# Kernel tuning notes

Measured on AMD Instinct MI355X. Metric: run time of the kernel, lower is better.

Reference implementation:

```python
import jax, jax.numpy as jnp
import numpy as np

PZ = 8            # pz half-patch in get_dist_base
P = 2 * PZ        # patch side = 16
C, T, HF, WF = 128, 3, 256, 256
N = 2048          # number of keypoint pairs


def setup_inputs() -> dict:
    key = jax.random.key(0)
    ks = jax.random.split(key, 9)
    response = jax.random.normal(ks[0], (C, T, HF, WF), dtype=jnp.float32)
    ys1 = jax.random.randint(ks[1], (N,), 0, HF - P, dtype=jnp.int32)
    xs1 = jax.random.randint(ks[2], (N,), 0, WF - P, dtype=jnp.int32)
    ts1 = jax.random.randint(ks[3], (N,), 0, T, dtype=jnp.int32)
    ys2 = jax.random.randint(ks[4], (N,), 0, HF - P, dtype=jnp.int32)
    xs2 = jax.random.randint(ks[5], (N,), 0, WF - P, dtype=jnp.int32)
    ts2 = jax.random.randint(ks[6], (N,), 0, T, dtype=jnp.int32)
    pair_type = jax.random.randint(ks[7], (N,), 0, 3, dtype=jnp.int32)  # 0=BG,1=I,2=IS
    powers = 1.0 + jax.random.uniform(ks[8], (3,), dtype=jnp.float32)   # per-type exponent in [1,2)
    plus = jnp.ones((1,), dtype=jnp.float32)
    return dict(response=response, ys1=ys1, xs1=xs1, ts1=ts1,
                ys2=ys2, xs2=xs2, ts2=ts2, pair_type=pair_type,
                powers=powers, plus=plus)


def _gather_patches(response, ts, ys, xs):
    # response: [C, T, Hf, Wf] -> patches [N, C, P, P]
    c = response.shape[0]
    def one(t, y, x):
        return jax.lax.dynamic_slice(response, (0, t, y, x), (c, 1, P, P))[:, 0]
    return jax.vmap(one)(ts, ys, xs)


def _minmax_norm(p):
    # normalize_tensor: min-max over whole patch; identity if max==min
    mn = p.min(axis=(1, 2, 3), keepdims=True)
    mx = p.max(axis=(1, 2, 3), keepdims=True)
    rng = mx - mn
    return jnp.where(rng != 0, (p - mn) / jnp.where(rng == 0, 1.0, rng), p)


def reference(response, ys1, xs1, ts1, ys2, xs2, ts2, pair_type, powers, plus):
    P1 = _minmax_norm(_gather_patches(response, ts1, ys1, xs1))
    P2 = _minmax_norm(_gather_patches(response, ts2, ys2, xs2))
    pw = powers[pair_type][:, None, None, None]            # per-pair exponent
    d = jnp.mean(jnp.abs(P1 - P2) ** pw, axis=(1, 2, 3))   # losscal core, [N]
    per = jnp.where(pair_type == 2, d, 1.0 / (1.0 + d))    # IS -> losscal_1, BG/I -> losscal_2
    per = per + jnp.where(pair_type == 0, 0.0, plus[0] * 0.5)  # + plus/2 for I and IS
    return jnp.mean(per)                                   # lossbase / act
```

## Files before the change

### kernel.cpp

```cpp
#include <hip/hip_runtime.h>
#include <math.h>

#define CC 128
#define TT 3
#define HFD 256
#define WFD 256
#define PP 16
#define NPAIR 2048
#define HW (HFD * WFD)
#define POS (TT * HW)
#define CH_STRIDE POS
#define PATCH_ELEMS (CC * PP * PP)
#define BLOCK 256
#define TP 256

typedef float floatx2 __attribute__((ext_vector_type(2)));
typedef float floatx4 __attribute__((ext_vector_type(4)));

__global__ __launch_bounds__(BLOCK) void transpose_minmax_kernel(
    const float* __restrict__ resp,
    unsigned int* __restrict__ rt32,
    float* __restrict__ cmn, float* __restrict__ cmx) {
    __shared__ unsigned int tile32[TP][33];
    __shared__ float smn[4][TP], smx[4][TP];

    int p0 = blockIdx.x * TP;
    int pc = threadIdx.x & 63;
    int ph = threadIdx.x >> 6;

    const float* bp = resp + p0 + 4 * pc;

    float mn0 = INFINITY, mn1 = INFINITY, mn2 = INFINITY, mn3 = INFINITY;
    float mx0 = -INFINITY, mx1 = -INFINITY, mx2 = -INFINITY, mx3 = -INFINITY;

    #pragma unroll
    for (int k = 0; k < 8; ++k) {
        int q = k * 4 + ph;
        floatx4 l0 = *(const floatx4*)(bp + (size_t)(4 * q + 0) * CH_STRIDE);
        floatx4 l1 = *(const floatx4*)(bp + (size_t)(4 * q + 1) * CH_STRIDE);
        floatx4 l2 = *(const floatx4*)(bp + (size_t)(4 * q + 2) * CH_STRIDE);
        floatx4 l3 = *(const floatx4*)(bp + (size_t)(4 * q + 3) * CH_STRIDE);
        #pragma unroll
        for (int j = 0; j < 4; ++j) {
            float v0 = l0[j], v1 = l1[j], v2 = l2[j], v3 = l3[j];
            float mnj = fminf(fminf(v0, v1), fminf(v2, v3));
            float mxj = fmaxf(fmaxf(v0, v1), fmaxf(v2, v3));
            if (j == 0) { mn0 = fminf(mn0, mnj); mx0 = fmaxf(mx0, mxj); }
            if (j == 1) { mn1 = fminf(mn1, mnj); mx1 = fmaxf(mx1, mxj); }
            if (j == 2) { mn2 = fminf(mn2, mnj); mx2 = fmaxf(mx2, mxj); }
            if (j == 3) { mn3 = fminf(mn3, mnj); mx3 = fmaxf(mx3, mxj); }
            int w = __builtin_amdgcn_cvt_pk_fp8_f32(v0, v1, 0, false);
            w = __builtin_amdgcn_cvt_pk_fp8_f32(v2, v3, w, true);
            tile32[4 * pc + j][q] = (unsigned int)w;
        }
    }
    smn[ph][4 * pc + 0] = mn0; smx[ph][4 * pc + 0] = mx0;
    smn[ph][4 * pc + 1] = mn1; smx[ph][4 * pc + 1] = mx1;
    smn[ph][4 * pc + 2] = mn2; smx[ph][4 * pc + 2] = mx2;
    smn[ph][4 * pc + 3] = mn3; smx[ph][4 * pc + 3] = mx3;
    __syncthreads();

    int tp = threadIdx.x;
    cmn[p0 + tp] = fminf(fminf(smn[0][tp], smn[1][tp]), fminf(smn[2][tp], smn[3][tp]));
    cmx[p0 + tp] = fmaxf(fmaxf(smx[0][tp], smx[1][tp]), fmaxf(smx[2][tp], smx[3][tp]));

    #pragma unroll
    for (int j = 0; j < 32; ++j) {
        int u   = j * BLOCK + threadIdx.x;
        int pos = u >> 5;
        int c4  = u & 31;
        rt32[(((size_t)(p0 + pos)) << 5) + c4] = tile32[pos][c4];
    }
}

__device__ inline float pw_term(float va, float vb, float sc1, float nsc2, float K, float pw) {
    float d = fmaf(va, sc1, fmaf(vb, nsc2, K));
    return __builtin_amdgcn_exp2f(pw * __builtin_amdgcn_logf(fabsf(d)));
}

__device__ inline float quad_acc(unsigned int wa, unsigned int wb,
                                 float sc1, float nsc2, float K, float pw) {
    floatx2 a0 = __builtin_amdgcn_cvt_pk_f32_fp8((int)wa, false);
    floatx2 a1 = __builtin_amdgcn_cvt_pk_f32_fp8((int)wa, true);
    floatx2 b0 = __builtin_amdgcn_cvt_pk_f32_fp8((int)wb, false);
    floatx2 b1 = __builtin_amdgcn_cvt_pk_f32_fp8((int)wb, true);
    return pw_term(a0.x, b0.x, sc1, nsc2, K, pw) + pw_term(a0.y, b0.y, sc1, nsc2, K, pw)
         + pw_term(a1.x, b1.x, sc1, nsc2, K, pw) + pw_term(a1.y, b1.y, sc1, nsc2, K, pw);
}

__global__ __launch_bounds__(BLOCK) void pair_loss_kernel(
    const uint4* __restrict__ rt,
    const int* __restrict__ ts1, const int* __restrict__ ys1, const int* __restrict__ xs1,
    const int* __restrict__ ts2, const int* __restrict__ ys2, const int* __restrict__ xs2,
    const int* __restrict__ pair_type,
    const float* __restrict__ powers,
    const float* __restrict__ plus,
    const float* __restrict__ cmn, const float* __restrict__ cmx,
    float* __restrict__ per_out) {
    int i = blockIdx.x;
    int t1 = ts1[i], y1 = ys1[i], x1 = xs1[i];
    int t2 = ts2[i], y2 = ys2[i], x2 = xs2[i];
    int p1 = t1 * HW + y1 * WFD + x1;
    int p2 = t2 * HW + y2 * WFD + x2;

    int dy = threadIdx.x >> 4, dx = threadIdx.x & 15;
    int q1 = p1 + dy * WFD + dx;
    int q2 = p2 + dy * WFD + dx;
    float a0 = cmn[q1], a1 = cmx[q1];
    float b0 = cmn[q2], b1 = cmx[q2];
    #pragma unroll
    for (int off = 32; off > 0; off >>= 1) {
        a0 = fminf(a0, __shfl_down(a0, off));
        a1 = fmaxf(a1, __shfl_down(a1, off));
        b0 = fminf(b0, __shfl_down(b0, off));
        b1 = fmaxf(b1, __shfl_down(b1, off));
    }
    __shared__ float red[4][4];
    int wave = threadIdx.x >> 6;
    if ((threadIdx.x & 63) == 0) {
        red[wave][0] = a0; red[wave][1] = a1; red[wave][2] = b0; red[wave][3] = b1;
    }
    __syncthreads();
    float mn1 = fminf(fminf(red[0][0], red[1][0]), fminf(red[2][0], red[3][0]));
    float mx1 = fmaxf(fmaxf(red[0][1], red[1][1]), fmaxf(red[2][1], red[3][1]));
    float mn2 = fminf(fminf(red[0][2], red[1][2]), fminf(red[2][2], red[3][2]));
    float mx2 = fmaxf(fmaxf(red[0][3], red[1][3]), fmaxf(red[2][3], red[3][3]));

    float rg1 = mx1 - mn1, rg2 = mx2 - mn2;
    float sc1 = (rg1 != 0.0f) ? (1.0f / rg1) : 1.0f;
    float sh1 = (rg1 != 0.0f) ? mn1 : 0.0f;
    float sc2 = (rg2 != 0.0f) ? (1.0f / rg2) : 1.0f;
    float sh2 = (rg2 != 0.0f) ? mn2 : 0.0f;
    float nsc2 = -sc2;
    float K = sh2 * sc2 - sh1 * sc1;

    int   ptype = pair_type[i];
    float pw    = powers[ptype];

    int c16 = threadIdx.x & 7;
    int pdx = (threadIdx.x >> 3) & 15;
    int dyb = threadIdx.x >> 7;
    const uint4* A = rt + (((size_t)(p1 + pdx)) << 3) + c16;
    const uint4* B = rt + (((size_t)(p2 + pdx)) << 3) + c16;
    const size_t RSTR = (size_t)WFD << 3;

    float acc = 0.0f;
    #pragma unroll
    for (int j = 0; j < 8; ++j) {
        size_t off = (size_t)(dyb + 2 * j) * RSTR;
        uint4 wa = A[off];
        uint4 wb = B[off];
        acc += quad_acc(wa.x, wb.x, sc1, nsc2, K, pw);
        acc += quad_acc(wa.y, wb.y, sc1, nsc2, K, pw);
        acc += quad_acc(wa.z, wb.z, sc1, nsc2, K, pw);
        acc += quad_acc(wa.w, wb.w, sc1, nsc2, K, pw);
    }
    for (int off = 32; off > 0; off >>= 1) acc += __shfl_down(acc, off);
    __shared__ float ssum[BLOCK / 64];
    if ((threadIdx.x & 63) == 0) ssum[wave] = acc;
    __syncthreads();
    if (threadIdx.x == 0) {
        float total = ssum[0] + ssum[1] + ssum[2] + ssum[3];
        float dmean = total * (1.0f / (float)PATCH_ELEMS);
        float per = (ptype == 2) ? dmean : (1.0f / (1.0f + dmean));
        per += (ptype == 0) ? 0.0f : plus[0] * 0.5f;
        per_out[i] = per;
    }
}

__global__ __launch_bounds__(BLOCK) void final_mean_kernel(
    const float* __restrict__ per_out, float* __restrict__ out) {
    float acc = 0.0f;
    for (int i = threadIdx.x; i < NPAIR; i += BLOCK) acc += per_out[i];
    for (int off = 32; off > 0; off >>= 1) acc += __shfl_down(acc, off);
    __shared__ float ssum[BLOCK / 64];
    int wave = threadIdx.x >> 6;
    if ((threadIdx.x & 63) == 0) ssum[wave] = acc;
    __syncthreads();
    if (threadIdx.x == 0) {
        float total = ssum[0] + ssum[1] + ssum[2] + ssum[3];
        out[0] = total * (1.0f / (float)NPAIR);
    }
}

extern "C" void kernel_launch(void* const* d_in, const int* in_sizes, int n_in,
                              void* d_out, int out_size, void* d_ws, size_t ws_size,
                              hipStream_t stream) {
    const float* resp      = (const float*)d_in[0];
    const int*   ys1       = (const int*)d_in[1];
    const int*   xs1       = (const int*)d_in[2];
    const int*   ts1       = (const int*)d_in[3];
    const int*   ys2       = (const int*)d_in[4];
    const int*   xs2       = (const int*)d_in[5];
    const int*   ts2       = (const int*)d_in[6];
    const int*   pair_type = (const int*)d_in[7];
    const float* powers    = (const float*)d_in[8];
    const float* plus      = (const float*)d_in[9];
    float*       out       = (float*)d_out;

    unsigned int* rt32 = (unsigned int*)d_ws;
    float* cmn     = (float*)(rt32 + (size_t)POS * 32);
    float* cmx     = cmn + POS;
    float* per_out = cmx + POS;

    transpose_minmax_kernel<<<POS / TP, BLOCK, 0, stream>>>(resp, rt32, cmn, cmx);

    pair_loss_kernel<<<NPAIR, BLOCK, 0, stream>>>(
        (const uint4*)rt32, ts1, ys1, xs1, ts2, ys2, xs2, pair_type, powers, plus,
        cmn, cmx, per_out);

    final_mean_kernel<<<1, BLOCK, 0, stream>>>(per_out, out);
}
```

Before: 192.6 us.

## Split pair blocks in half, shrink transpose tile, hoist loads, precompute powers

The transpose/minmax kernel now works on 128-position tiles, which doubles its block count and gives each thread fewer channel loads. The pair kernel launches two blocks per pair, each covering half the patch rows. Each block issues its patch loads before the min/max reduction, with a sched barrier to keep them early. Per-pair exponents are precomputed by a small extra kernel, and the final per-pair combine moves into the final mean kernel. A stray dead load of cmn is left in, and the extra launch and partial-sum traffic add overhead.

```diff
diff --git a/kernel.cpp b/kernel.cpp
--- a/kernel.cpp
+++ b/kernel.cpp
@@ -12,7 +12,7 @@
 #define CH_STRIDE POS
 #define PATCH_ELEMS (CC * PP * PP)
 #define BLOCK 256
-#define TP 256
+#define TP 128
 
 typedef float floatx2 __attribute__((ext_vector_type(2)));
 typedef float floatx4 __attribute__((ext_vector_type(4)));
@@ -22,11 +22,11 @@
     unsigned int* __restrict__ rt32,
     float* __restrict__ cmn, float* __restrict__ cmx) {
     __shared__ unsigned int tile32[TP][33];
-    __shared__ float smn[4][TP], smx[4][TP];
+    __shared__ float smn[8][TP], smx[8][TP];
 
     int p0 = blockIdx.x * TP;
-    int pc = threadIdx.x & 63;
-    int ph = threadIdx.x >> 6;
+    int pc = threadIdx.x & 31;
+    int ph = threadIdx.x >> 5;
 
     const float* bp = resp + p0 + 4 * pc;
 
@@ -34,8 +34,8 @@
     float mx0 = -INFINITY, mx1 = -INFINITY, mx2 = -INFINITY, mx3 = -INFINITY;
 
     #pragma unroll
-    for (int k = 0; k < 8; ++k) {
-        int q = k * 4 + ph;
+    for (int k = 0; k < 4; ++k) {
+        int q = k * 8 + ph;
         floatx4 l0 = *(const floatx4*)(bp + (size_t)(4 * q + 0) * CH_STRIDE);
         floatx4 l1 = *(const floatx4*)(bp + (size_t)(4 * q + 1) * CH_STRIDE);
         floatx4 l2 = *(const floatx4*)(bp + (size_t)(4 * q + 2) * CH_STRIDE);
@@ -60,12 +60,20 @@
     smn[ph][4 * pc + 3] = mn3; smx[ph][4 * pc + 3] = mx3;
     __syncthreads();
 
-    int tp = threadIdx.x;
-    cmn[p0 + tp] = fminf(fminf(smn[0][tp], smn[1][tp]), fminf(smn[2][tp], smn[3][tp]));
-    cmx[p0 + tp] = fmaxf(fmaxf(smx[0][tp], smx[1][tp]), fmaxf(smx[2][tp], smx[3][tp]));
-
-    #pragma unroll
-    for (int j = 0; j < 32; ++j) {
+    if (threadIdx.x < TP) {
+        int tp = threadIdx.x;
+        float mn = smn[0][tp], mx = smx[0][tp];
+        #pragma unroll
+        for (int h = 1; h < 8; ++h) {
+            mn = fminf(mn, smn[h][tp]);
+            mx = fmaxf(mx, smx[h][tp]);
+        }
+        cmn[p0 + tp] = mn;
+        cmx[p0 + tp] = mx;
+    }
+
+    #pragma unroll
+    for (int j = 0; j < 16; ++j) {
         int u   = j * BLOCK + threadIdx.x;
         int pos = u >> 5;
         int c4  = u & 31;
@@ -92,16 +100,29 @@
     const uint4* __restrict__ rt,
     const int* __restrict__ ts1, const int* __restrict__ ys1, const int* __restrict__ xs1,
     const int* __restrict__ ts2, const int* __restrict__ ys2, const int* __restrict__ xs2,
-    const int* __restrict__ pair_type,
-    const float* __restrict__ powers,
-    const float* __restrict__ plus,
     const float* __restrict__ cmn, const float* __restrict__ cmx,
-    float* __restrict__ per_out) {
-    int i = blockIdx.x;
+    float* __restrict__ part) {
+    int i  = blockIdx.x >> 1;
+    int hf = blockIdx.x & 1;
     int t1 = ts1[i], y1 = ys1[i], x1 = xs1[i];
     int t2 = ts2[i], y2 = ys2[i], x2 = xs2[i];
     int p1 = t1 * HW + y1 * WFD + x1;
     int p2 = t2 * HW + y2 * WFD + x2;
+
+    int c16 = threadIdx.x & 7;
+    int pdx = (threadIdx.x >> 3) & 15;
+    int dyq = threadIdx.x >> 7;
+    const size_t RSTR = (size_t)WFD << 3;
+    const uint4* A = rt + (((size_t)(p1 + pdx)) << 3) + c16 + (size_t)(hf * 8 + dyq) * RSTR;
+    const uint4* B = rt + (((size_t)(p2 + pdx)) << 3) + c16 + (size_t)(hf * 8 + dyq) * RSTR;
+
+    uint4 wa[4], wb[4];
+    #pragma unroll
+    for (int j = 0; j < 4; ++j) {
+        wa[j] = A[(size_t)(2 * j) * RSTR];
+        wb[j] = B[(size_t)(2 * j) * RSTR];
+    }
+    __builtin_amdgcn_sched_barrier(0);
 
     int dy = threadIdx.x >> 4, dx = threadIdx.x & 15;
     int q1 = p1 + dy * WFD + dx;
@@ -133,45 +154,49 @@
     float sh2 = (rg2 != 0.0f) ? mn2 : 0.0f;
     float nsc2 = -sc2;
     float K = sh2 * sc2 - sh1 * sc1;
-
-    int   ptype = pair_type[i];
-    float pw    = powers[ptype];
-
-    int c16 = threadIdx.x & 7;
-    int pdx = (threadIdx.x >> 3) & 15;
-    int dyb = threadIdx.x >> 7;
-    const uint4* A = rt + (((size_t)(p1 + pdx)) << 3) + c16;
-    const uint4* B = rt + (((size_t)(p2 + pdx)) << 3) + c16;
-    const size_t RSTR = (size_t)WFD << 3;
-
+    float pw = *(const float*)((const char*)cmn - 0);
+    ;
     float acc = 0.0f;
-    #pragma unroll
-    for (int j = 0; j < 8; ++j) {
-        size_t off = (size_t)(dyb + 2 * j) * RSTR;
-        uint4 wa = A[off];
-        uint4 wb = B[off];
-        acc += quad_acc(wa.x, wb.x, sc1, nsc2, K, pw);
-        acc += quad_acc(wa.y, wb.y, sc1, nsc2, K, pw);
-        acc += quad_acc(wa.z, wb.z, sc1, nsc2, K, pw);
-        acc += quad_acc(wa.w, wb.w, sc1, nsc2, K, pw);
+    {
+    }
+    const float* powers_by_pair = part + 2 * NPAIR;
+    float pwv = powers_by_pair[i];
+    #pragma unroll
+    for (int j = 0; j < 4; ++j) {
+        acc += quad_acc(wa[j].x, wb[j].x, sc1, nsc2, K, pwv);
+        acc += quad_acc(wa[j].y, wb[j].y, sc1, nsc2, K, pwv);
+        acc += quad_acc(wa[j].z, wb[j].z, sc1, nsc2, K, pwv);
+        acc += quad_acc(wa[j].w, wb[j].w, sc1, nsc2, K, pwv);
     }
     for (int off = 32; off > 0; off >>= 1) acc += __shfl_down(acc, off);
     __shared__ float ssum[BLOCK / 64];
     if ((threadIdx.x & 63) == 0) ssum[wave] = acc;
     __syncthreads();
     if (threadIdx.x == 0) {
-        float total = ssum[0] + ssum[1] + ssum[2] + ssum[3];
+        part[2 * i + hf] = ssum[0] + ssum[1] + ssum[2] + ssum[3];
+    }
+}
+
+__global__ __launch_bounds__(BLOCK) void setup_pw_kernel(
+    const int* __restrict__ pair_type, const float* __restrict__ powers,
+    float* __restrict__ powers_by_pair) {
+    int i = blockIdx.x * BLOCK + threadIdx.x;
+    if (i < NPAIR) powers_by_pair[i] = powers[pair_type[i]];
+}
+
+__global__ __launch_bounds__(BLOCK) void final_mean_kernel(
+    const float* __restrict__ part, const int* __restrict__ pair_type,
+    const float* __restrict__ plus, float* __restrict__ out) {
+    float acc = 0.0f;
+    float pl = plus[0] * 0.5f;
+    for (int i = threadIdx.x; i < NPAIR; i += BLOCK) {
+        float total = part[2 * i] + part[2 * i + 1];
         float dmean = total * (1.0f / (float)PATCH_ELEMS);
+        int ptype = pair_type[i];
         float per = (ptype == 2) ? dmean : (1.0f / (1.0f + dmean));
-        per += (ptype == 0) ? 0.0f : plus[0] * 0.5f;
-        per_out[i] = per;
-    }
-}
-
-__global__ __launch_bounds__(BLOCK) void final_mean_kernel(
-    const float* __restrict__ per_out, float* __restrict__ out) {
-    float acc = 0.0f;
-    for (int i = threadIdx.x; i < NPAIR; i += BLOCK) acc += per_out[i];
+        per += (ptype == 0) ? 0.0f : pl;
+        acc += per;
+    }
     for (int off = 32; off > 0; off >>= 1) acc += __shfl_down(acc, off);
     __shared__ float ssum[BLOCK / 64];
     int wave = threadIdx.x >> 6;
@@ -199,15 +224,17 @@
     float*       out       = (float*)d_out;
 
     unsigned int* rt32 = (unsigned int*)d_ws;
-    float* cmn     = (float*)(rt32 + (size_t)POS * 32);
-    float* cmx     = cmn + POS;
-    float* per_out = cmx + POS;
+    float* cmn  = (float*)(rt32 + (size_t)POS * 32);
+    float* cmx  = cmn + POS;
+    float* part = cmx + POS;
+
+    setup_pw_kernel<<<(NPAIR + BLOCK - 1) / BLOCK, BLOCK, 0, stream>>>(
+        pair_type, powers, part + 2 * NPAIR);
 
     transpose_minmax_kernel<<<POS / TP, BLOCK, 0, stream>>>(resp, rt32, cmn, cmx);
 
-    pair_loss_kernel<<<NPAIR, BLOCK, 0, stream>>>(
-        (const uint4*)rt32, ts1, ys1, xs1, ts2, ys2, xs2, pair_type, powers, plus,
-        cmn, cmx, per_out);
-
-    final_mean_kernel<<<1, BLOCK, 0, stream>>>(per_out, out);
-}
+    pair_loss_kernel<<<2 * NPAIR, BLOCK, 0, stream>>>(
+        (const uint4*)rt32, ts1, ys1, xs1, ts2, ys2, xs2, cmn, cmx, part);
+
+    final_mean_kernel<<<1, BLOCK, 0, stream>>>(part, pair_type, plus, out);
+}
```

Measured after the change: 200.7 us. 4.2% more time.
